# Kernel tuning notes

Hardware: AMD Instinct MI355X
Metric: run time of the kernel (lower is better)

Reference implementation:

```python
import jax, jax.numpy as jnp
import numpy as np

LATENT = 32
HIDDEN = 512
NUM_LAYERS = 3  # number of hidden activations before the final tanh layer
BATCH = 512

# layer dims: latent -> hidden -> hidden -> hidden -> latent (num_layers=3)
DIMS = [LATENT] + [HIDDEN] * NUM_LAYERS + [LATENT]
PARAM_COUNT = sum(do * di + do for di, do in zip(DIMS[:-1], DIMS[1:]))  # 558624


def setup_inputs() -> dict:
    key = jax.random.key(0)
    k1, k2 = jax.random.split(key)
    z = jax.random.normal(k1, (BATCH, LATENT), dtype=jnp.float32)
    # hypernet weights are init'd Normal(0, 0.01); its output params are small
    params = jax.random.normal(k2, (BATCH, PARAM_COUNT), dtype=jnp.float32) * 0.02
    t = jnp.float32(0.0)
    return {"t": t, "z": z, "params": params}


def reference(t, z, params):
    """Per-sample-weight MLP: weights sliced from flat params vector per sample.
    Matches torch flat-param layout: per Linear, weight [out,in] row-major, then bias.
    """
    B = z.shape[0]
    h = z
    off = 0
    n = len(DIMS) - 1
    for i in range(n):
        din, dout = DIMS[i], DIMS[i + 1]
        W = params[:, off:off + dout * din].reshape(B, dout, din)
        off += dout * din
        b = params[:, off:off + dout]
        off += dout
        h = jnp.einsum('boi,bi->bo', W, h) + b
        h = jnp.tanh(h) if i == n - 1 else jax.nn.silu(h)
    return h
```

## Files before the change

### kernel.cpp

```cpp
#include <hip/hip_runtime.h>
#include <math.h>


#define BATCH  512
#define LATENT 32
#define HIDDEN 512
#define PCOUNT 558624

#define W1_OFF 0
#define B1_OFF 16384
#define W2_OFF 16896
#define B2_OFF 279040
#define W3_OFF 279552
#define B3_OFF 541696
#define W4_OFF 542208
#define B4_OFF 558592

__device__ __forceinline__ float silu_f(float x) {
    return x / (1.0f + expf(-x));
}

__device__ __forceinline__ float dot4(float4 a, float4 b) {
    return a.x * b.x + a.y * b.y + a.z * b.z + a.w * b.w;
}

__device__ __forceinline__ float wsum64(float v) {
    v += __shfl_xor(v, 1);
    v += __shfl_xor(v, 2);
    v += __shfl_xor(v, 4);
    v += __shfl_xor(v, 8);
    v += __shfl_xor(v, 16);
    v += __shfl_xor(v, 32);
    return v;
}

__device__ __forceinline__ void layer512(const float* __restrict__ W,
                                         const float* __restrict__ bvec,
                                         const float* __restrict__ hin_lds,
                                         float* __restrict__ hout_lds,
                                         int wave, int lane) {
    float4 ha = *(const float4*)(hin_lds + 4 * lane);
    float4 hb = *(const float4*)(hin_lds + 256 + 4 * lane);
    const float* Wp = W + (size_t)wave * 64 * 512 + 4 * lane;
    const int o0 = wave * 64;
    for (int it = 0; it < 16; ++it) {
        const float* q = Wp + (size_t)it * 4 * 512;
        float4 a0 = *(const float4*)(q);
        float4 b0 = *(const float4*)(q + 256);
        float4 a1 = *(const float4*)(q + 512);
        float4 b1 = *(const float4*)(q + 768);
        float4 a2 = *(const float4*)(q + 1024);
        float4 b2 = *(const float4*)(q + 1280);
        float4 a3 = *(const float4*)(q + 1536);
        float4 b3 = *(const float4*)(q + 1792);
        float s0 = wsum64(dot4(a0, ha) + dot4(b0, hb));
        float s1 = wsum64(dot4(a1, ha) + dot4(b1, hb));
        float s2 = wsum64(dot4(a2, ha) + dot4(b2, hb));
        float s3 = wsum64(dot4(a3, ha) + dot4(b3, hb));
        if (lane < 4) {
            int o = o0 + it * 4 + lane;
            float s = (lane == 0) ? s0 : (lane == 1) ? s1 : (lane == 2) ? s2 : s3;
            hout_lds[o] = silu_f(s + bvec[o]);
        }
    }
}

__global__ __launch_bounds__(512) void mlp_kernel(const float* __restrict__ z,
                                                  const float* __restrict__ params,
                                                  float* __restrict__ out) {
    const int b    = blockIdx.x;
    const int tid  = threadIdx.x;
    const int wave = tid >> 6;
    const int lane = tid & 63;

    const float* __restrict__ p = params + (size_t)b * PCOUNT;

    __shared__ __align__(16) float hA[HIDDEN];
    __shared__ __align__(16) float hB[HIDDEN];

    {
        const int j = lane & 7;
        const int r = lane >> 3;
        float4 zin = *(const float4*)(z + b * LATENT + 4 * j);
        #pragma unroll
        for (int it = 0; it < 8; ++it) {
            int o = wave * 64 + it * 8 + r;
            float4 w = *(const float4*)(p + W1_OFF + (size_t)o * LATENT + 4 * j);
            float acc = dot4(w, zin);
            acc += __shfl_xor(acc, 1);
            acc += __shfl_xor(acc, 2);
            acc += __shfl_xor(acc, 4);
            if (j == 0) {
                hA[o] = silu_f(acc + p[B1_OFF + o]);
            }
        }
    }
    __syncthreads();

    layer512(p + W2_OFF, p + B2_OFF, hA, hB, wave, lane);
    __syncthreads();

    layer512(p + W3_OFF, p + B3_OFF, hB, hA, wave, lane);
    __syncthreads();

    {
        float4 ha = *(const float4*)(hA + 4 * lane);
        float4 hb = *(const float4*)(hA + 256 + 4 * lane);
        const float* q = p + W4_OFF + (size_t)wave * 4 * 512 + 4 * lane;
        float4 a0 = *(const float4*)(q);
        float4 b0 = *(const float4*)(q + 256);
        float4 a1 = *(const float4*)(q + 512);
        float4 b1 = *(const float4*)(q + 768);
        float4 a2 = *(const float4*)(q + 1024);
        float4 b2 = *(const float4*)(q + 1280);
        float4 a3 = *(const float4*)(q + 1536);
        float4 b3 = *(const float4*)(q + 1792);
        float s0 = wsum64(dot4(a0, ha) + dot4(b0, hb));
        float s1 = wsum64(dot4(a1, ha) + dot4(b1, hb));
        float s2 = wsum64(dot4(a2, ha) + dot4(b2, hb));
        float s3 = wsum64(dot4(a3, ha) + dot4(b3, hb));
        if (lane < 4) {
            int o = wave * 4 + lane;
            float s = (lane == 0) ? s0 : (lane == 1) ? s1 : (lane == 2) ? s2 : s3;
            out[(size_t)b * LATENT + o] = tanhf(s + p[B4_OFF + o]);
        }
    }
}

extern "C" void kernel_launch(void* const* d_in, const int* in_sizes, int n_in,
                              void* d_out, int out_size, void* d_ws, size_t ws_size,
                              hipStream_t stream) {
    const float* z      = (const float*)d_in[1];
    const float* params = (const float*)d_in[2];
    float* out          = (float*)d_out;
    mlp_kernel<<<BATCH, 512, 0, stream>>>(z, params, out);
}
```

Before: 1.397 ms.

## Use 16-lane row groups with register double-buffered weight prefetch

```diff
diff --git a/kernel.cpp b/kernel.cpp
--- a/kernel.cpp
+++ b/kernel.cpp
@@ -20,54 +20,64 @@
     return x / (1.0f + expf(-x));
 }
 
-__device__ __forceinline__ float dot4(float4 a, float4 b) {
-    return a.x * b.x + a.y * b.y + a.z * b.z + a.w * b.w;
-}
-
-__device__ __forceinline__ float wsum64(float v) {
-    v += __shfl_xor(v, 1);
-    v += __shfl_xor(v, 2);
-    v += __shfl_xor(v, 4);
-    v += __shfl_xor(v, 8);
-    v += __shfl_xor(v, 16);
-    v += __shfl_xor(v, 32);
-    return v;
+__device__ __forceinline__ float acc4(float4 w, float4 h, float a) {
+    a = fmaf(w.x, h.x, a);
+    a = fmaf(w.y, h.y, a);
+    a = fmaf(w.z, h.z, a);
+    a = fmaf(w.w, h.w, a);
+    return a;
 }
 
 __device__ __forceinline__ void layer512(const float* __restrict__ W,
                                          const float* __restrict__ bvec,
-                                         const float* __restrict__ hin_lds,
-                                         float* __restrict__ hout_lds,
+                                         const float* __restrict__ hin,
+                                         float* __restrict__ hout,
                                          int wave, int lane) {
-    float4 ha = *(const float4*)(hin_lds + 4 * lane);
-    float4 hb = *(const float4*)(hin_lds + 256 + 4 * lane);
-    const float* Wp = W + (size_t)wave * 64 * 512 + 4 * lane;
-    const int o0 = wave * 64;
+    const int g = lane >> 4;
+    const int s = lane & 15;
+
+    float4 hv[8];
+    #pragma unroll
+    for (int k = 0; k < 8; ++k)
+        hv[k] = *(const float4*)(hin + k * 64 + s * 4);
+
+    const int r0 = wave * 64 + g;
+    const float* __restrict__ Wp = W + (size_t)r0 * 512 + s * 4;
+
+    float4 wb[2][8];
+    #pragma unroll
+    for (int k = 0; k < 8; ++k)
+        wb[0][k] = *(const float4*)(Wp + k * 64);
+
+    #pragma unroll
     for (int it = 0; it < 16; ++it) {
-        const float* q = Wp + (size_t)it * 4 * 512;
-        float4 a0 = *(const float4*)(q);
-        float4 b0 = *(const float4*)(q + 256);
-        float4 a1 = *(const float4*)(q + 512);
-        float4 b1 = *(const float4*)(q + 768);
-        float4 a2 = *(const float4*)(q + 1024);
-        float4 b2 = *(const float4*)(q + 1280);
-        float4 a3 = *(const float4*)(q + 1536);
-        float4 b3 = *(const float4*)(q + 1792);
-        float s0 = wsum64(dot4(a0, ha) + dot4(b0, hb));
-        float s1 = wsum64(dot4(a1, ha) + dot4(b1, hb));
-        float s2 = wsum64(dot4(a2, ha) + dot4(b2, hb));
-        float s3 = wsum64(dot4(a3, ha) + dot4(b3, hb));
-        if (lane < 4) {
-            int o = o0 + it * 4 + lane;
-            float s = (lane == 0) ? s0 : (lane == 1) ? s1 : (lane == 2) ? s2 : s3;
-            hout_lds[o] = silu_f(s + bvec[o]);
+        if (it < 15) {
+            const float* __restrict__ Wn = Wp + (size_t)(it + 1) * 2048;
+            #pragma unroll
+            for (int k = 0; k < 8; ++k)
+                wb[(it + 1) & 1][k] = *(const float4*)(Wn + k * 64);
+        }
+        float a0 = 0.0f, a1 = 0.0f;
+        #pragma unroll
+        for (int k = 0; k < 8; k += 2) {
+            a0 = acc4(wb[it & 1][k],     hv[k],     a0);
+            a1 = acc4(wb[it & 1][k + 1], hv[k + 1], a1);
+        }
+        float acc = a0 + a1;
+        acc += __shfl_xor(acc, 1);
+        acc += __shfl_xor(acc, 2);
+        acc += __shfl_xor(acc, 4);
+        acc += __shfl_xor(acc, 8);
+        if (s == 0) {
+            const int o = r0 + it * 4;
+            hout[o] = silu_f(acc + bvec[o]);
         }
     }
 }
 
-__global__ __launch_bounds__(512) void mlp_kernel(const float* __restrict__ z,
-                                                  const float* __restrict__ params,
-                                                  float* __restrict__ out) {
+__global__ __launch_bounds__(512, 4) void mlp_kernel(const float* __restrict__ z,
+                                                     const float* __restrict__ params,
+                                                     float* __restrict__ out) {
     const int b    = blockIdx.x;
     const int tid  = threadIdx.x;
     const int wave = tid >> 6;
@@ -86,7 +96,7 @@
         for (int it = 0; it < 8; ++it) {
             int o = wave * 64 + it * 8 + r;
             float4 w = *(const float4*)(p + W1_OFF + (size_t)o * LATENT + 4 * j);
-            float acc = dot4(w, zin);
+            float acc = acc4(w, zin, 0.0f);
             acc += __shfl_xor(acc, 1);
             acc += __shfl_xor(acc, 2);
             acc += __shfl_xor(acc, 4);
@@ -104,25 +114,27 @@
     __syncthreads();
 
     {
-        float4 ha = *(const float4*)(hA + 4 * lane);
-        float4 hb = *(const float4*)(hA + 256 + 4 * lane);
-        const float* q = p + W4_OFF + (size_t)wave * 4 * 512 + 4 * lane;
-        float4 a0 = *(const float4*)(q);
-        float4 b0 = *(const float4*)(q + 256);
-        float4 a1 = *(const float4*)(q + 512);
-        float4 b1 = *(const float4*)(q + 768);
-        float4 a2 = *(const float4*)(q + 1024);
-        float4 b2 = *(const float4*)(q + 1280);
-        float4 a3 = *(const float4*)(q + 1536);
-        float4 b3 = *(const float4*)(q + 1792);
-        float s0 = wsum64(dot4(a0, ha) + dot4(b0, hb));
-        float s1 = wsum64(dot4(a1, ha) + dot4(b1, hb));
-        float s2 = wsum64(dot4(a2, ha) + dot4(b2, hb));
-        float s3 = wsum64(dot4(a3, ha) + dot4(b3, hb));
-        if (lane < 4) {
-            int o = wave * 4 + lane;
-            float s = (lane == 0) ? s0 : (lane == 1) ? s1 : (lane == 2) ? s2 : s3;
-            out[(size_t)b * LATENT + o] = tanhf(s + p[B4_OFF + o]);
+        const int g = lane >> 4;
+        const int s = lane & 15;
+        float4 hv[8];
+        #pragma unroll
+        for (int k = 0; k < 8; ++k)
+            hv[k] = *(const float4*)(hA + k * 64 + s * 4);
+        const int row = wave * 4 + g;
+        const float* __restrict__ q = p + W4_OFF + (size_t)row * 512 + s * 4;
+        float a0 = 0.0f, a1 = 0.0f;
+        #pragma unroll
+        for (int k = 0; k < 8; k += 2) {
+            a0 = acc4(*(const float4*)(q + k * 64),       hv[k],     a0);
+            a1 = acc4(*(const float4*)(q + (k + 1) * 64), hv[k + 1], a1);
+        }
+        float acc = a0 + a1;
+        acc += __shfl_xor(acc, 1);
+        acc += __shfl_xor(acc, 2);
+        acc += __shfl_xor(acc, 4);
+        acc += __shfl_xor(acc, 8);
+        if (s == 0) {
+            out[(size_t)b * LATENT + row] = tanhf(acc + p[B4_OFF + row]);
         }
     }
 }
```

Measured after the change: 1.398 ms. Within noise of the previous version (+0.1%).
